# Kernel tuning notes

Hardware: AMD Instinct MI355X
Metric: run time of the kernel (lower is better)

The kernel has to match this reference:

```python
import jax, jax.numpy as jnp
import numpy as np

F_FIELDS, HH, WW = 17, 300, 400   # hardcoded cifhr buffer in __init__
H_F, W_F = 38, 50                 # field grid: ~hr_size / stride
STRIDE = 8
V_TH = 0.1
NEIGHBORS = 16
MIN_SCALE = 0.0
FACTOR = 1.0
R = 13                            # window half-width; covers 2*sigma_max = 12 truncation radius


def _approx_exp(x):
    # openpifpaf fast exp approximation; only evaluated for x in [-2, 0]
    y = 1.0 + x / 8.0
    y = y * y
    y = y * y
    y = y * y
    return y


def _accumulate(cifhr, field):
    # field: (F, 5, H_f, W_f) with channels [confidence, x_reg, y_reg, b, scale]
    F = field.shape[0]
    v = field[:, 0]                        # (F,H,W)
    px = field[:, 1] * STRIDE              # hr-grid x position
    py = field[:, 2] * STRIDE              # hr-grid y position
    scale = field[:, 4]
    sigma = jnp.maximum(1.0, 0.5 * scale * STRIDE)
    value = v / NEIGHBORS * FACTOR
    valid = (v >= V_TH) & (scale * STRIDE >= MIN_SCALE)

    cx = jnp.round(px).astype(jnp.int32)
    cy = jnp.round(py).astype(jnp.int32)
    offs = jnp.arange(-R, R + 1, dtype=jnp.int32)   # (K,)
    xx = cx[..., None] + offs                        # (F,H,W,K)
    yy = cy[..., None] + offs                        # (F,H,W,K)
    dx2 = (xx.astype(px.dtype) - px[..., None]) ** 2  # (F,H,W,K)
    dy2 = (yy.astype(py.dtype) - py[..., None]) ** 2  # (F,H,W,K)
    d2 = dy2[..., :, None] + dx2[..., None, :]       # (F,H,W,K,K) y-major
    sigma2 = (sigma ** 2)[..., None, None]
    trunc2 = 4.0 * sigma2                            # truncate = 2*sigma
    inb = ((yy >= 0) & (yy < HH))[..., :, None] & ((xx >= 0) & (xx < WW))[..., None, :]
    mask = (d2 <= trunc2) & inb & valid[..., None, None]
    nearest = (dy2[..., :, None] < 0.25) & (dx2[..., None, :] < 0.25)
    g = jnp.where(nearest, 1.0, _approx_exp(-0.5 * d2 / sigma2))
    contrib = jnp.where(mask, value[..., None, None] * g, 0.0)

    fidx = jnp.arange(F, dtype=jnp.int32)[:, None, None, None, None]
    yc = jnp.clip(yy[..., :, None], 0, HH - 1)
    xc = jnp.clip(xx[..., None, :], 0, WW - 1)
    flat_idx = (fidx * HH + yc) * WW + xc            # (F,H,W,K,K)
    out = cifhr.reshape(-1).at[flat_idx.reshape(-1)].add(contrib.reshape(-1))
    return jnp.minimum(out.reshape(F_FIELDS, HH, WW), 1.0)


def setup_inputs() -> dict:
    key = jax.random.key(0)
    k1, k2, k3, k4, k5 = jax.random.split(key, 5)
    cifhr = jnp.zeros((F_FIELDS, HH, WW), dtype=jnp.float32)
    # confidence in [0,1]
    conf = jax.random.uniform(k1, (F_FIELDS, 1, H_F, W_F), dtype=jnp.float32)
    gx = jnp.broadcast_to(jnp.arange(W_F, dtype=jnp.float32)[None, None, None, :],
                          (F_FIELDS, 1, H_F, W_F))
    gy = jnp.broadcast_to(jnp.arange(H_F, dtype=jnp.float32)[None, None, :, None],
                          (F_FIELDS, 1, H_F, W_F))
    xr = gx + 0.5 * jax.random.normal(k2, (F_FIELDS, 1, H_F, W_F), dtype=jnp.float32)
    yr = gy + 0.5 * jax.random.normal(k3, (F_FIELDS, 1, H_F, W_F), dtype=jnp.float32)
    b = jax.random.uniform(k4, (F_FIELDS, 1, H_F, W_F), dtype=jnp.float32)
    # scale in [0.5, 1.5] -> sigma = max(1, 0.5*scale*stride) <= 6
    scale = 0.5 + jax.random.uniform(k5, (F_FIELDS, 1, H_F, W_F), dtype=jnp.float32)
    x = jnp.concatenate([conf, xr, yr, b, scale], axis=1)  # (17,5,38,50)
    return {"cifhr": cifhr, "x": x}


def reference(cifhr, x):
    return _accumulate(cifhr, x)
```

## Files before the change

### kernel.cpp

```cpp
#include <hip/hip_runtime.h>
#include <hip/hip_bf16.h>
#include <stdint.h>

#define F_FIELDS 17
#define HH 300
#define WW 400
#define H_F 38
#define W_F 50
#define PTS_PER_FIELD (H_F * W_F)
#define RAD 13

#define GX 13
#define GY 10
#define CAP 80

__global__ __launch_bounds__(256) void cifhr_fused_kernel(
    const float* __restrict__ x, const float* __restrict__ cifhr,
    float* __restrict__ out) {
    __shared__ float4 sA[4][CAP];
    __shared__ float  sB[4][CAP];
    __shared__ int    cnt[4];

    const int tid = threadIdx.x;
    const int f = blockIdx.z;
    const int X0 = blockIdx.x * 32;
    const int Y0 = blockIdx.y * 32;
    const int sxmax = min(1, (WW - 1 - X0) >> 4);
    const int symax = min(1, (HH - 1 - Y0) >> 4);
    const int xvhi = X0 + ((sxmax + 1) << 4) - 1;
    const int yvhi = Y0 + ((symax + 1) << 4) - 1;

    if (tid < 4) cnt[tid] = 0;
    __syncthreads();

    const float* base = x + (size_t)(f * 5) * PTS_PER_FIELD;
    for (int p = tid; p < PTS_PER_FIELD; p += 256) {
        float v  = base[p];
        float xr = base[PTS_PER_FIELD + p];
        float yr = base[2 * PTS_PER_FIELD + p];
        float sc = base[4 * PTS_PER_FIELD + p];
        if (!(v >= 0.1f) || !(sc * 8.0f >= 0.0f)) continue;
        float px = xr * 8.0f;
        float py = yr * 8.0f;
        int cx = (int)rintf(px);
        int cy = (int)rintf(py);
        float sigma  = fmaxf(1.0f, 4.0f * sc);
        float sigma2 = sigma * sigma;
        int rp = min(RAD, (int)(2.0f * sigma + 0.5f));
        int xlo = cx - rp, xhi = cx + rp;
        int ylo = cy - rp, yhi = cy + rp;
        if (xhi < X0 || xlo > xvhi || yhi < Y0 || ylo > yvhi) continue;
        int sx0 = max(0, (xlo - X0) >> 4), sx1 = min(sxmax, (xhi - X0) >> 4);
        int sy0 = max(0, (ylo - Y0) >> 4), sy1 = min(symax, (yhi - Y0) >> 4);
        float4 rec = make_float4(px, py, v * 0.0625f, -1.0f / (16.0f * sigma2));
        float tr = 4.0f * sigma2;
        for (int sy = sy0; sy <= sy1; ++sy)
            for (int sx = sx0; sx <= sx1; ++sx) {
                int s = sy * 2 + sx;
                int slot = atomicAdd(&cnt[s], 1);
                if (slot < CAP) { sA[s][slot] = rec; sB[s][slot] = tr; }
            }
    }
    __syncthreads();

    const int s  = tid >> 6;
    const int ln = tid & 63;
    const int sx = s & 1, sy = s >> 1;
    if (sx > sxmax || sy > symax) return;

    const int xb = X0 + (sx << 4) + ((ln & 7) << 1);
    const int yb = Y0 + (sy << 4) + ((ln >> 3) << 1);
    const float xf0 = (float)xb,  xf1 = (float)(xb + 1);
    const float yf0 = (float)yb,  yf1 = (float)(yb + 1);

    const int n = min(cnt[s], CAP);
    float a00 = 0.0f, a01 = 0.0f, a10 = 0.0f, a11 = 0.0f;
    for (int k = 0; k < n; ++k) {
        float4 a = sA[s][k];
        float tr = sB[s][k];
        float dx0 = xf0 - a.x, dx1 = xf1 - a.x;
        float dy0 = yf0 - a.y, dy1 = yf1 - a.y;
        float dx0s = dx0 * dx0, dx1s = dx1 * dx1;
        float dy0s = dy0 * dy0, dy1s = dy1 * dy1;
        {
            float d2 = dy0s + dx0s;
            float t8 = fmaf(a.w, d2, 1.0f); t8 *= t8; t8 *= t8; t8 *= t8;
            float g  = (fmaxf(dy0s, dx0s) < 0.25f) ? 1.0f : t8;
            a00 += (d2 <= tr) ? a.z * g : 0.0f;
        }
        {
            float d2 = dy0s + dx1s;
            float t8 = fmaf(a.w, d2, 1.0f); t8 *= t8; t8 *= t8; t8 *= t8;
            float g  = (fmaxf(dy0s, dx1s) < 0.25f) ? 1.0f : t8;
            a01 += (d2 <= tr) ? a.z * g : 0.0f;
        }
        {
            float d2 = dy1s + dx0s;
            float t8 = fmaf(a.w, d2, 1.0f); t8 *= t8; t8 *= t8; t8 *= t8;
            float g  = (fmaxf(dy1s, dx0s) < 0.25f) ? 1.0f : t8;
            a10 += (d2 <= tr) ? a.z * g : 0.0f;
        }
        {
            float d2 = dy1s + dx1s;
            float t8 = fmaf(a.w, d2, 1.0f); t8 *= t8; t8 *= t8; t8 *= t8;
            float g  = (fmaxf(dy1s, dx1s) < 0.25f) ? 1.0f : t8;
            a11 += (d2 <= tr) ? a.z * g : 0.0f;
        }
    }

    if (yb < HH) {
        size_t idx = ((size_t)f * HH + yb) * WW + xb;
        const float2 c = *(const float2*)(cifhr + idx);
        float2 o;
        o.x = fminf(a00 + c.x, 1.0f);
        o.y = fminf(a01 + c.y, 1.0f);
        *(float2*)(out + idx) = o;
    }
    if (yb + 1 < HH) {
        size_t idx = ((size_t)f * HH + yb + 1) * WW + xb;
        const float2 c = *(const float2*)(cifhr + idx);
        float2 o;
        o.x = fminf(a10 + c.x, 1.0f);
        o.y = fminf(a11 + c.y, 1.0f);
        *(float2*)(out + idx) = o;
    }
}

extern "C" void kernel_launch(void* const* d_in, const int* in_sizes, int n_in,
                              void* d_out, int out_size, void* d_ws, size_t ws_size,
                              hipStream_t stream) {
    const float* cifhr = (const float*)d_in[0];
    const float* x     = (const float*)d_in[1];
    float* out = (float*)d_out;

    dim3 grid(GX, GY, F_FIELDS);
    cifhr_fused_kernel<<<grid, 256, 0, stream>>>(x, cifhr, out);
}
```

Baseline: 79.71 us.

## Split fused kernel into global binning pass plus per-tile gather kernel

Replaces the per-block redundant scan of all field points with a separate binning kernel that scatters each point once into global per-tile lists via atomics, followed by a gather kernel that loads each tile's list into shared memory and evaluates the gaussian sum. This removes the cost of every block rereading and filtering all 1900 points of its field, at the price of a memset, two extra launches, and global atomics and workspace traffic. CAP drops from 80 to 64, which could truncate dense tiles. A fallback to the original fused kernel is kept when the workspace is too small.

```diff
diff --git a/kernel.cpp b/kernel.cpp
--- a/kernel.cpp
+++ b/kernel.cpp
@@ -1,5 +1,4 @@
 #include <hip/hip_runtime.h>
-#include <hip/hip_bf16.h>
 #include <stdint.h>
 
 #define F_FIELDS 17
@@ -8,19 +7,137 @@
 #define H_F 38
 #define W_F 50
 #define PTS_PER_FIELD (H_F * W_F)
+#define NPTS (F_FIELDS * PTS_PER_FIELD)
 #define RAD 13
 
+#define TX 25
+#define TY 19
+#define NTILES (TX * TY * F_FIELDS)
+#define CAP 64
 #define GX 13
 #define GY 10
-#define CAP 80
-
+
+#define OFF_CNT  ((size_t)0)
+#define OFF_A    ((size_t)32768)
+#define OFF_B    (OFF_A + (size_t)NTILES * CAP * 16)
+#define WS_NEEDED (OFF_B + (size_t)NTILES * CAP * 4)
+
+__global__ __launch_bounds__(64) void cifhr_bin_kernel(
+    const float* __restrict__ x, int* __restrict__ cnt,
+    float4* __restrict__ A, float* __restrict__ B) {
+    int p = blockIdx.x * 64 + threadIdx.x;
+    if (p >= NPTS) return;
+    int f = p / PTS_PER_FIELD;
+    int ij = p - f * PTS_PER_FIELD;
+    const float* base = x + (size_t)(f * 5) * PTS_PER_FIELD + ij;
+    float v  = base[0];
+    float xr = base[PTS_PER_FIELD];
+    float yr = base[2 * PTS_PER_FIELD];
+    float sc = base[4 * PTS_PER_FIELD];
+    if (!(v >= 0.1f) || !(sc * 8.0f >= 0.0f)) return;
+    float px = xr * 8.0f;
+    float py = yr * 8.0f;
+    int cx = (int)rintf(px);
+    int cy = (int)rintf(py);
+    float sigma  = fmaxf(1.0f, 4.0f * sc);
+    float sigma2 = sigma * sigma;
+    int rp = min(RAD, (int)(2.0f * sigma + 0.5f));
+    int sx0 = max(0, (cx - rp) >> 4), sx1 = min(TX - 1, (cx + rp) >> 4);
+    int sy0 = max(0, (cy - rp) >> 4), sy1 = min(TY - 1, (cy + rp) >> 4);
+    float4 rec = make_float4(px, py, v * 0.0625f, -1.0f / (16.0f * sigma2));
+    float tr = 4.0f * sigma2;
+    for (int sy = sy0; sy <= sy1; ++sy)
+        for (int sx = sx0; sx <= sx1; ++sx) {
+            int t = (f * TY + sy) * TX + sx;
+            int slot = atomicAdd(&cnt[t], 1);
+            if (slot < CAP) {
+                A[(size_t)t * CAP + slot] = rec;
+                B[(size_t)t * CAP + slot] = tr;
+            }
+        }
+}
+
+__global__ __launch_bounds__(256) void cifhr_gather_kernel(
+    const int* __restrict__ cnt, const float4* __restrict__ A,
+    const float* __restrict__ B, const float* __restrict__ cifhr,
+    float* __restrict__ out) {
+    __shared__ float4 sA[4][CAP];
+    __shared__ float  sB[4][CAP];
+
+    const int tid = threadIdx.x;
+    const int s = tid >> 6, ln = tid & 63;
+    const int f = blockIdx.z;
+    const int sx = blockIdx.x * 2 + (s & 1);
+    const int sy = blockIdx.y * 2 + (s >> 1);
+    const bool active = (sx < TX) && (sy < TY);
+
+    int n = 0, t = 0;
+    if (active) {
+        t = (f * TY + sy) * TX + sx;
+        n = min(cnt[t], CAP);
+        if (ln < n) {
+            sA[s][ln] = A[(size_t)t * CAP + ln];
+            sB[s][ln] = B[(size_t)t * CAP + ln];
+        }
+    }
+    __syncthreads();
+    if (!active) return;
+
+    const int xb = (sx << 4) + ((ln & 7) << 1);
+    const int yb = (sy << 4) + ((ln >> 3) << 1);
+    const float xf0 = (float)xb, xf1 = (float)(xb + 1);
+    const float yf0 = (float)yb, yf1 = (float)(yb + 1);
+
+    const bool w0 = (yb < HH), w1 = (yb + 1 < HH);
+    const size_t idx0 = ((size_t)f * HH + yb) * WW + xb;
+    const size_t idx1 = idx0 + WW;
+    float2 c0 = w0 ? *(const float2*)(cifhr + idx0) : make_float2(0.f, 0.f);
+    float2 c1 = w1 ? *(const float2*)(cifhr + idx1) : make_float2(0.f, 0.f);
+
+    float a00 = 0.0f, a01 = 0.0f, a10 = 0.0f, a11 = 0.0f;
+    #pragma unroll 2
+    for (int k = 0; k < n; ++k) {
+        float4 a = sA[s][k];
+        float tr = sB[s][k];
+        float dx0 = xf0 - a.x, dx1 = xf1 - a.x;
+        float dy0 = yf0 - a.y, dy1 = yf1 - a.y;
+        float dx0s = dx0 * dx0, dx1s = dx1 * dx1;
+        float dy0s = dy0 * dy0, dy1s = dy1 * dy1;
+        {   float d2 = dy0s + dx0s;
+            float t8 = fmaf(a.w, d2, 1.0f); t8 *= t8; t8 *= t8; t8 *= t8;
+            float g  = (fmaxf(dy0s, dx0s) < 0.25f) ? 1.0f : t8;
+            a00 += (d2 <= tr) ? a.z * g : 0.0f; }
+        {   float d2 = dy0s + dx1s;
+            float t8 = fmaf(a.w, d2, 1.0f); t8 *= t8; t8 *= t8; t8 *= t8;
+            float g  = (fmaxf(dy0s, dx1s) < 0.25f) ? 1.0f : t8;
+            a01 += (d2 <= tr) ? a.z * g : 0.0f; }
+        {   float d2 = dy1s + dx0s;
+            float t8 = fmaf(a.w, d2, 1.0f); t8 *= t8; t8 *= t8; t8 *= t8;
+            float g  = (fmaxf(dy1s, dx0s) < 0.25f) ? 1.0f : t8;
+            a10 += (d2 <= tr) ? a.z * g : 0.0f; }
+        {   float d2 = dy1s + dx1s;
+            float t8 = fmaf(a.w, d2, 1.0f); t8 *= t8; t8 *= t8; t8 *= t8;
+            float g  = (fmaxf(dy1s, dx1s) < 0.25f) ? 1.0f : t8;
+            a11 += (d2 <= tr) ? a.z * g : 0.0f; }
+    }
+
+    if (w0) {
+        float2 o; o.x = fminf(a00 + c0.x, 1.0f); o.y = fminf(a01 + c0.y, 1.0f);
+        *(float2*)(out + idx0) = o;
+    }
+    if (w1) {
+        float2 o; o.x = fminf(a10 + c1.x, 1.0f); o.y = fminf(a11 + c1.y, 1.0f);
+        *(float2*)(out + idx1) = o;
+    }
+}
+
+#define FCAP 80
 __global__ __launch_bounds__(256) void cifhr_fused_kernel(
     const float* __restrict__ x, const float* __restrict__ cifhr,
     float* __restrict__ out) {
-    __shared__ float4 sA[4][CAP];
-    __shared__ float  sB[4][CAP];
+    __shared__ float4 sA[4][FCAP];
+    __shared__ float  sB[4][FCAP];
     __shared__ int    cnt[4];
-
     const int tid = threadIdx.x;
     const int f = blockIdx.z;
     const int X0 = blockIdx.x * 32;
@@ -29,10 +146,8 @@
     const int symax = min(1, (HH - 1 - Y0) >> 4);
     const int xvhi = X0 + ((sxmax + 1) << 4) - 1;
     const int yvhi = Y0 + ((symax + 1) << 4) - 1;
-
     if (tid < 4) cnt[tid] = 0;
     __syncthreads();
-
     const float* base = x + (size_t)(f * 5) * PTS_PER_FIELD;
     for (int p = tid; p < PTS_PER_FIELD; p += 256) {
         float v  = base[p];
@@ -40,15 +155,12 @@
         float yr = base[2 * PTS_PER_FIELD + p];
         float sc = base[4 * PTS_PER_FIELD + p];
         if (!(v >= 0.1f) || !(sc * 8.0f >= 0.0f)) continue;
-        float px = xr * 8.0f;
-        float py = yr * 8.0f;
-        int cx = (int)rintf(px);
-        int cy = (int)rintf(py);
+        float px = xr * 8.0f, py = yr * 8.0f;
+        int cx = (int)rintf(px), cy = (int)rintf(py);
         float sigma  = fmaxf(1.0f, 4.0f * sc);
         float sigma2 = sigma * sigma;
         int rp = min(RAD, (int)(2.0f * sigma + 0.5f));
-        int xlo = cx - rp, xhi = cx + rp;
-        int ylo = cy - rp, yhi = cy + rp;
+        int xlo = cx - rp, xhi = cx + rp, ylo = cy - rp, yhi = cy + rp;
         if (xhi < X0 || xlo > xvhi || yhi < Y0 || ylo > yvhi) continue;
         int sx0 = max(0, (xlo - X0) >> 4), sx1 = min(sxmax, (xhi - X0) >> 4);
         int sy0 = max(0, (ylo - Y0) >> 4), sy1 = min(symax, (yhi - Y0) >> 4);
@@ -56,25 +168,21 @@
         float tr = 4.0f * sigma2;
         for (int sy = sy0; sy <= sy1; ++sy)
             for (int sx = sx0; sx <= sx1; ++sx) {
-                int s = sy * 2 + sx;
-                int slot = atomicAdd(&cnt[s], 1);
-                if (slot < CAP) { sA[s][slot] = rec; sB[s][slot] = tr; }
+                int sidx = sy * 2 + sx;
+                int slot = atomicAdd(&cnt[sidx], 1);
+                if (slot < FCAP) { sA[sidx][slot] = rec; sB[sidx][slot] = tr; }
             }
     }
     __syncthreads();
-
-    const int s  = tid >> 6;
-    const int ln = tid & 63;
+    const int s  = tid >> 6, ln = tid & 63;
     const int sx = s & 1, sy = s >> 1;
     if (sx > sxmax || sy > symax) return;
-
     const int xb = X0 + (sx << 4) + ((ln & 7) << 1);
     const int yb = Y0 + (sy << 4) + ((ln >> 3) << 1);
-    const float xf0 = (float)xb,  xf1 = (float)(xb + 1);
-    const float yf0 = (float)yb,  yf1 = (float)(yb + 1);
-
-    const int n = min(cnt[s], CAP);
-    float a00 = 0.0f, a01 = 0.0f, a10 = 0.0f, a11 = 0.0f;
+    const float xf0 = (float)xb, xf1 = (float)(xb + 1);
+    const float yf0 = (float)yb, yf1 = (float)(yb + 1);
+    const int n = min(cnt[s], FCAP);
+    float a00 = 0, a01 = 0, a10 = 0, a11 = 0;
     for (int k = 0; k < n; ++k) {
         float4 a = sA[s][k];
         float tr = sB[s][k];
@@ -82,46 +190,33 @@
         float dy0 = yf0 - a.y, dy1 = yf1 - a.y;
         float dx0s = dx0 * dx0, dx1s = dx1 * dx1;
         float dy0s = dy0 * dy0, dy1s = dy1 * dy1;
-        {
-            float d2 = dy0s + dx0s;
-            float t8 = fmaf(a.w, d2, 1.0f); t8 *= t8; t8 *= t8; t8 *= t8;
-            float g  = (fmaxf(dy0s, dx0s) < 0.25f) ? 1.0f : t8;
-            a00 += (d2 <= tr) ? a.z * g : 0.0f;
-        }
-        {
-            float d2 = dy0s + dx1s;
-            float t8 = fmaf(a.w, d2, 1.0f); t8 *= t8; t8 *= t8; t8 *= t8;
-            float g  = (fmaxf(dy0s, dx1s) < 0.25f) ? 1.0f : t8;
-            a01 += (d2 <= tr) ? a.z * g : 0.0f;
-        }
-        {
-            float d2 = dy1s + dx0s;
-            float t8 = fmaf(a.w, d2, 1.0f); t8 *= t8; t8 *= t8; t8 *= t8;
-            float g  = (fmaxf(dy1s, dx0s) < 0.25f) ? 1.0f : t8;
-            a10 += (d2 <= tr) ? a.z * g : 0.0f;
-        }
-        {
-            float d2 = dy1s + dx1s;
-            float t8 = fmaf(a.w, d2, 1.0f); t8 *= t8; t8 *= t8; t8 *= t8;
-            float g  = (fmaxf(dy1s, dx1s) < 0.25f) ? 1.0f : t8;
-            a11 += (d2 <= tr) ? a.z * g : 0.0f;
-        }
-    }
-
+        { float d2 = dy0s + dx0s; float t8 = fmaf(a.w, d2, 1.0f);
+          t8 *= t8; t8 *= t8; t8 *= t8;
+          float g = (fmaxf(dy0s, dx0s) < 0.25f) ? 1.0f : t8;
+          a00 += (d2 <= tr) ? a.z * g : 0.0f; }
+        { float d2 = dy0s + dx1s; float t8 = fmaf(a.w, d2, 1.0f);
+          t8 *= t8; t8 *= t8; t8 *= t8;
+          float g = (fmaxf(dy0s, dx1s) < 0.25f) ? 1.0f : t8;
+          a01 += (d2 <= tr) ? a.z * g : 0.0f; }
+        { float d2 = dy1s + dx0s; float t8 = fmaf(a.w, d2, 1.0f);
+          t8 *= t8; t8 *= t8; t8 *= t8;
+          float g = (fmaxf(dy1s, dx0s) < 0.25f) ? 1.0f : t8;
+          a10 += (d2 <= tr) ? a.z * g : 0.0f; }
+        { float d2 = dy1s + dx1s; float t8 = fmaf(a.w, d2, 1.0f);
+          t8 *= t8; t8 *= t8; t8 *= t8;
+          float g = (fmaxf(dy1s, dx1s) < 0.25f) ? 1.0f : t8;
+          a11 += (d2 <= tr) ? a.z * g : 0.0f; }
+    }
     if (yb < HH) {
         size_t idx = ((size_t)f * HH + yb) * WW + xb;
         const float2 c = *(const float2*)(cifhr + idx);
-        float2 o;
-        o.x = fminf(a00 + c.x, 1.0f);
-        o.y = fminf(a01 + c.y, 1.0f);
+        float2 o; o.x = fminf(a00 + c.x, 1.0f); o.y = fminf(a01 + c.y, 1.0f);
         *(float2*)(out + idx) = o;
     }
     if (yb + 1 < HH) {
         size_t idx = ((size_t)f * HH + yb + 1) * WW + xb;
         const float2 c = *(const float2*)(cifhr + idx);
-        float2 o;
-        o.x = fminf(a10 + c.x, 1.0f);
-        o.y = fminf(a11 + c.y, 1.0f);
+        float2 o; o.x = fminf(a10 + c.x, 1.0f); o.y = fminf(a11 + c.y, 1.0f);
         *(float2*)(out + idx) = o;
     }
 }
@@ -133,6 +228,17 @@
     const float* x     = (const float*)d_in[1];
     float* out = (float*)d_out;
 
-    dim3 grid(GX, GY, F_FIELDS);
-    cifhr_fused_kernel<<<grid, 256, 0, stream>>>(x, cifhr, out);
-}
+    if (ws_size >= WS_NEEDED) {
+        char* ws = (char*)d_ws;
+        int*    cnt = (int*)(ws + OFF_CNT);
+        float4* A   = (float4*)(ws + OFF_A);
+        float*  B   = (float*)(ws + OFF_B);
+        hipMemsetAsync(cnt, 0, (size_t)NTILES * sizeof(int), stream);
+        cifhr_bin_kernel<<<(NPTS + 63) / 64, 64, 0, stream>>>(x, cnt, A, B);
+        dim3 grid(GX, GY, F_FIELDS);
+        cifhr_gather_kernel<<<grid, 256, 0, stream>>>(cnt, A, B, cifhr, out);
+    } else {
+        dim3 grid(GX, GY, F_FIELDS);
+        cifhr_fused_kernel<<<grid, 256, 0, stream>>>(x, cifhr, out);
+    }
+}
```

New measurement: 85.63 us. 1.07x slower.

## Software-pipeline field loads and broadcast splat records via readlane

Applied to the files above, without the earlier changes.

The binning loop now prefetches the next iteration's field values before processing the current point, an 8-step unrolled software pipeline. In the accumulation loop each lane loads one splat record from LDS once, and all lanes then read record k through readlane instead of repeated LDS reads. The cifhr loads are hoisted ahead of the compute loop so their latency is hidden. CAP drops from 80 to 64 to match the 64-lane wavefront, which truncates tiles that collect more than 64 splats and could change results in dense regions.

```diff
diff --git a/kernel.cpp b/kernel.cpp
--- a/kernel.cpp
+++ b/kernel.cpp
@@ -1,5 +1,4 @@
 #include <hip/hip_runtime.h>
-#include <hip/hip_bf16.h>
 #include <stdint.h>
 
 #define F_FIELDS 17
@@ -12,7 +11,11 @@
 
 #define GX 13
 #define GY 10
-#define CAP 80
+#define CAP 64
+
+__device__ __forceinline__ float bcast(float v, int k) {
+    return __int_as_float(__builtin_amdgcn_readlane(__float_as_int(v), k));
+}
 
 __global__ __launch_bounds__(256) void cifhr_fused_kernel(
     const float* __restrict__ x, const float* __restrict__ cifhr,
@@ -34,95 +37,109 @@
     __syncthreads();
 
     const float* base = x + (size_t)(f * 5) * PTS_PER_FIELD;
-    for (int p = tid; p < PTS_PER_FIELD; p += 256) {
-        float v  = base[p];
-        float xr = base[PTS_PER_FIELD + p];
-        float yr = base[2 * PTS_PER_FIELD + p];
-        float sc = base[4 * PTS_PER_FIELD + p];
-        if (!(v >= 0.1f) || !(sc * 8.0f >= 0.0f)) continue;
-        float px = xr * 8.0f;
-        float py = yr * 8.0f;
-        int cx = (int)rintf(px);
-        int cy = (int)rintf(py);
-        float sigma  = fmaxf(1.0f, 4.0f * sc);
-        float sigma2 = sigma * sigma;
-        int rp = min(RAD, (int)(2.0f * sigma + 0.5f));
-        int xlo = cx - rp, xhi = cx + rp;
-        int ylo = cy - rp, yhi = cy + rp;
-        if (xhi < X0 || xlo > xvhi || yhi < Y0 || ylo > yvhi) continue;
-        int sx0 = max(0, (xlo - X0) >> 4), sx1 = min(sxmax, (xhi - X0) >> 4);
-        int sy0 = max(0, (ylo - Y0) >> 4), sy1 = min(symax, (yhi - Y0) >> 4);
-        float4 rec = make_float4(px, py, v * 0.0625f, -1.0f / (16.0f * sigma2));
-        float tr = 4.0f * sigma2;
-        for (int sy = sy0; sy <= sy1; ++sy)
-            for (int sx = sx0; sx <= sx1; ++sx) {
-                int s = sy * 2 + sx;
-                int slot = atomicAdd(&cnt[s], 1);
-                if (slot < CAP) { sA[s][slot] = rec; sB[s][slot] = tr; }
+    int   p0 = tid;
+    bool  ok0 = (p0 < PTS_PER_FIELD);
+    float v0 = 0.f, xr0 = 0.f, yr0 = 0.f, sc0 = 0.f;
+    if (ok0) {
+        v0  = base[p0];
+        xr0 = base[PTS_PER_FIELD + p0];
+        yr0 = base[2 * PTS_PER_FIELD + p0];
+        sc0 = base[4 * PTS_PER_FIELD + p0];
+    }
+    #pragma unroll
+    for (int i = 0; i < 8; ++i) {
+        int   p1 = p0 + 256;
+        bool  ok1 = (p1 < PTS_PER_FIELD);
+        float v1 = 0.f, xr1 = 0.f, yr1 = 0.f, sc1 = 0.f;
+        if (ok1) {
+            v1  = base[p1];
+            xr1 = base[PTS_PER_FIELD + p1];
+            yr1 = base[2 * PTS_PER_FIELD + p1];
+            sc1 = base[4 * PTS_PER_FIELD + p1];
+        }
+        if (ok0 && (v0 >= 0.1f) && (sc0 * 8.0f >= 0.0f)) {
+            float px = xr0 * 8.0f;
+            float py = yr0 * 8.0f;
+            int cx = (int)rintf(px);
+            int cy = (int)rintf(py);
+            float sigma  = fmaxf(1.0f, 4.0f * sc0);
+            float sigma2 = sigma * sigma;
+            int rp = min(RAD, (int)(2.0f * sigma + 0.5f));
+            int xlo = cx - rp, xhi = cx + rp;
+            int ylo = cy - rp, yhi = cy + rp;
+            if (!(xhi < X0 || xlo > xvhi || yhi < Y0 || ylo > yvhi)) {
+                int sx0 = max(0, (xlo - X0) >> 4), sx1 = min(sxmax, (xhi - X0) >> 4);
+                int sy0 = max(0, (ylo - Y0) >> 4), sy1 = min(symax, (yhi - Y0) >> 4);
+                float4 rec = make_float4(px, py, v0 * 0.0625f,
+                                         -1.0f / (16.0f * sigma2));
+                float tr = 4.0f * sigma2;
+                for (int sy = sy0; sy <= sy1; ++sy)
+                    for (int sx = sx0; sx <= sx1; ++sx) {
+                        int sidx = sy * 2 + sx;
+                        int slot = atomicAdd(&cnt[sidx], 1);
+                        if (slot < CAP) { sA[sidx][slot] = rec; sB[sidx][slot] = tr; }
+                    }
             }
+        }
+        p0 = p1; ok0 = ok1; v0 = v1; xr0 = xr1; yr0 = yr1; sc0 = sc1;
     }
     __syncthreads();
 
-    const int s  = tid >> 6;
-    const int ln = tid & 63;
+    const int s  = tid >> 6, ln = tid & 63;
     const int sx = s & 1, sy = s >> 1;
     if (sx > sxmax || sy > symax) return;
 
+    const int n = min(cnt[s], CAP);
+    float4 mya = sA[s][ln];
+    float  myt = sB[s][ln];
+
     const int xb = X0 + (sx << 4) + ((ln & 7) << 1);
     const int yb = Y0 + (sy << 4) + ((ln >> 3) << 1);
-    const float xf0 = (float)xb,  xf1 = (float)(xb + 1);
-    const float yf0 = (float)yb,  yf1 = (float)(yb + 1);
+    const float xf0 = (float)xb, xf1 = (float)(xb + 1);
+    const float yf0 = (float)yb, yf1 = (float)(yb + 1);
 
-    const int n = min(cnt[s], CAP);
+    const bool w0 = (yb < HH), w1 = (yb + 1 < HH);
+    const size_t idx0 = ((size_t)f * HH + yb) * WW + xb;
+    const size_t idx1 = idx0 + WW;
+    float2 c0 = w0 ? *(const float2*)(cifhr + idx0) : make_float2(0.f, 0.f);
+    float2 c1 = w1 ? *(const float2*)(cifhr + idx1) : make_float2(0.f, 0.f);
+
     float a00 = 0.0f, a01 = 0.0f, a10 = 0.0f, a11 = 0.0f;
     for (int k = 0; k < n; ++k) {
-        float4 a = sA[s][k];
-        float tr = sB[s][k];
-        float dx0 = xf0 - a.x, dx1 = xf1 - a.x;
-        float dy0 = yf0 - a.y, dy1 = yf1 - a.y;
+        float ax = bcast(mya.x, k);
+        float ay = bcast(mya.y, k);
+        float az = bcast(mya.z, k);
+        float aw = bcast(mya.w, k);
+        float tr = bcast(myt,   k);
+        float dx0 = xf0 - ax, dx1 = xf1 - ax;
+        float dy0 = yf0 - ay, dy1 = yf1 - ay;
         float dx0s = dx0 * dx0, dx1s = dx1 * dx1;
         float dy0s = dy0 * dy0, dy1s = dy1 * dy1;
-        {
-            float d2 = dy0s + dx0s;
-            float t8 = fmaf(a.w, d2, 1.0f); t8 *= t8; t8 *= t8; t8 *= t8;
+        {   float d2 = dy0s + dx0s;
+            float t8 = fmaf(aw, d2, 1.0f); t8 *= t8; t8 *= t8; t8 *= t8;
             float g  = (fmaxf(dy0s, dx0s) < 0.25f) ? 1.0f : t8;
-            a00 += (d2 <= tr) ? a.z * g : 0.0f;
-        }
-        {
-            float d2 = dy0s + dx1s;
-            float t8 = fmaf(a.w, d2, 1.0f); t8 *= t8; t8 *= t8; t8 *= t8;
+            a00 += (d2 <= tr) ? az * g : 0.0f; }
+        {   float d2 = dy0s + dx1s;
+            float t8 = fmaf(aw, d2, 1.0f); t8 *= t8; t8 *= t8; t8 *= t8;
             float g  = (fmaxf(dy0s, dx1s) < 0.25f) ? 1.0f : t8;
-            a01 += (d2 <= tr) ? a.z * g : 0.0f;
-        }
-        {
-            float d2 = dy1s + dx0s;
-            float t8 = fmaf(a.w, d2, 1.0f); t8 *= t8; t8 *= t8; t8 *= t8;
+            a01 += (d2 <= tr) ? az * g : 0.0f; }
+        {   float d2 = dy1s + dx0s;
+            float t8 = fmaf(aw, d2, 1.0f); t8 *= t8; t8 *= t8; t8 *= t8;
             float g  = (fmaxf(dy1s, dx0s) < 0.25f) ? 1.0f : t8;
-            a10 += (d2 <= tr) ? a.z * g : 0.0f;
-        }
-        {
-            float d2 = dy1s + dx1s;
-            float t8 = fmaf(a.w, d2, 1.0f); t8 *= t8; t8 *= t8; t8 *= t8;
+            a10 += (d2 <= tr) ? az * g : 0.0f; }
+        {   float d2 = dy1s + dx1s;
+            float t8 = fmaf(aw, d2, 1.0f); t8 *= t8; t8 *= t8; t8 *= t8;
             float g  = (fmaxf(dy1s, dx1s) < 0.25f) ? 1.0f : t8;
-            a11 += (d2 <= tr) ? a.z * g : 0.0f;
-        }
+            a11 += (d2 <= tr) ? az * g : 0.0f; }
     }
 
-    if (yb < HH) {
-        size_t idx = ((size_t)f * HH + yb) * WW + xb;
-        const float2 c = *(const float2*)(cifhr + idx);
-        float2 o;
-        o.x = fminf(a00 + c.x, 1.0f);
-        o.y = fminf(a01 + c.y, 1.0f);
-        *(float2*)(out + idx) = o;
+    if (w0) {
+        float2 o; o.x = fminf(a00 + c0.x, 1.0f); o.y = fminf(a01 + c0.y, 1.0f);
+        *(float2*)(out + idx0) = o;
     }
-    if (yb + 1 < HH) {
-        size_t idx = ((size_t)f * HH + yb + 1) * WW + xb;
-        const float2 c = *(const float2*)(cifhr + idx);
-        float2 o;
-        o.x = fminf(a10 + c.x, 1.0f);
-        o.y = fminf(a11 + c.y, 1.0f);
-        *(float2*)(out + idx) = o;
+    if (w1) {
+        float2 o; o.x = fminf(a10 + c1.x, 1.0f); o.y = fminf(a11 + c1.y, 1.0f);
+        *(float2*)(out + idx1) = o;
     }
 }
 
```

Measured after the change: 78.68 us. About the same (-1.3%).
